# Kernel optimization log

Hardware: AMD Instinct MI355X
Metric: run time of the kernel (lower is better)

## Reference

```python
import jax, jax.numpy as jnp
import numpy as np

B, D = 8192, 1024
HR, HE, HF = 512, 4096, 2048
N_OPS, N_TASKS = 4, 4

def setup_inputs() -> dict:
    key = jax.random.key(0)
    ks = jax.random.split(key, 20)
    s = 0.02
    return {
        "x":        jax.random.normal(ks[0], (B, D), jnp.float32),
        # router
        "W_r1":   s*jax.random.normal(ks[1], (D, HR), jnp.float32),
        "b_r1":     jnp.zeros((HR,), jnp.float32),
        "W_dom":  s*jax.random.normal(ks[2], (HR, 2), jnp.float32),
        "b_dom":    jnp.zeros((2,), jnp.float32),
        "W_mop":  s*jax.random.normal(ks[3], (HR, N_OPS), jnp.float32),
        "W_lt":   s*jax.random.normal(ks[4], (HR, N_TASKS), jnp.float32),
        # math expert (operation hint = additive embedding)
        "op_emb": s*jax.random.normal(ks[5], (N_OPS, D), jnp.float32),
        "W_m1":   s*jax.random.normal(ks[6], (D, HE), jnp.float32),
        "b_m1":     jnp.zeros((HE,), jnp.float32),
        "W_m2":   s*jax.random.normal(ks[7], (HE, D), jnp.float32),
        "b_m2":     jnp.zeros((D,), jnp.float32),
        # language expert (task hint = additive embedding)
        "task_emb": s*jax.random.normal(ks[8], (N_TASKS, D), jnp.float32),
        "W_l1":   s*jax.random.normal(ks[9], (D, HE), jnp.float32),
        "b_l1":     jnp.zeros((HE,), jnp.float32),
        "W_l2":   s*jax.random.normal(ks[10], (HE, D), jnp.float32),
        "b_l2":     jnp.zeros((D,), jnp.float32),
        # fusion
        "W_f1":   s*jax.random.normal(ks[11], (D, HF), jnp.float32),
        "b_f1":     jnp.zeros((HF,), jnp.float32),
        "W_f2":   s*jax.random.normal(ks[12], (HF, D), jnp.float32),
        "b_f2":     jnp.zeros((D,), jnp.float32),
    }

def reference(x, W_r1, b_r1, W_dom, b_dom, W_mop, W_lt,
              op_emb, W_m1, b_m1, W_m2, b_m2,
              task_emb, W_l1, b_l1, W_l2, b_l2,
              W_f1, b_f1, W_f2, b_f2):
    # --- router ---
    h = jax.nn.relu(x @ W_r1 + b_r1)                      # [B, HR]
    dom_logits = h @ W_dom + b_dom                        # [B, 2]
    expert_weights = jax.nn.softmax(dom_logits, axis=-1)  # [B, 2]
    primary = jnp.argmax(dom_logits, axis=-1)             # [B]
    math_op = jnp.argmax(h @ W_mop, axis=-1)              # [B]
    lang_task = jnp.argmax(h @ W_lt, axis=-1)             # [B]
    # --- experts (vectorized equivalent of per-sample dispatch) ---
    math_in = x + op_emb[math_op]                         # [B, D]
    math_out = jax.nn.relu(math_in @ W_m1 + b_m1) @ W_m2 + b_m2
    lang_in = x + task_emb[lang_task]                     # [B, D]
    lang_out = jax.nn.relu(lang_in @ W_l1 + b_l1) @ W_l2 + b_l2
    selected = jnp.where((primary == 0)[:, None], math_out, lang_out)  # [B, D]
    # --- fusion: scale by routing weight of the chosen expert + MLP residual ---
    w = jnp.take_along_axis(expert_weights, primary[:, None], axis=1)  # [B, 1]
    fused = w * selected
    final = fused + jax.nn.relu(fused @ W_f1 + b_f1) @ W_f2 + b_f2     # [B, D]
    return final
```

## Files before the change

kernel.cpp:

```cpp
#include <hip/hip_runtime.h>
#include <hip/hip_bf16.h>
#include <stdint.h>

#define NB 8192
#define DD 1024
#define HRD 512
#define HED 4096
#define HFD 2048

typedef __attribute__((ext_vector_type(8))) short bf16x8;
typedef __attribute__((ext_vector_type(4))) float f32x4;
typedef unsigned short u16;

__device__ __forceinline__ u16 f2b(float f) {
    union { float f; uint32_t i; } c; c.f = f;
    uint32_t r = c.i + 0x7FFF + ((c.i >> 16) & 1);
    return (u16)(r >> 16);
}
__device__ __forceinline__ float b2f(u16 u) {
    union { uint32_t i; float f; } c; c.i = ((uint32_t)u) << 16; return c.f;
}

__device__ __forceinline__ void xcd_swz(int flat, int nwg, int nFast, int& f, int& s) {
    int xcd = flat & 7, rest = flat >> 3;
    int q = nwg >> 3, r = nwg & 7;
    int wg = (xcd < r ? xcd * (q + 1) : r * (q + 1) + (xcd - r) * q) + rest;
    f = wg % nFast; s = wg / nFast;
}

__global__ void k_init(int* cnt) { if (threadIdx.x < 2) cnt[threadIdx.x] = 0; }

__global__ __launch_bounds__(256) void k_split(const float4* __restrict__ x4,
                                               ushort4* __restrict__ hi4,
                                               ushort4* __restrict__ lo4) {
    int i = blockIdx.x * 256 + threadIdx.x;
    float4 v = x4[i];
    ushort4 h, l;
    h.x = f2b(v.x); l.x = f2b(v.x - b2f(h.x));
    h.y = f2b(v.y); l.y = f2b(v.y - b2f(h.y));
    h.z = f2b(v.z); l.z = f2b(v.z - b2f(h.z));
    h.w = f2b(v.w); l.w = f2b(v.w - b2f(h.w));
    hi4[i] = h; lo4[i] = l;
}

__global__ __launch_bounds__(256) void k_transpose(const float* __restrict__ in,
                                                   u16* __restrict__ out, int R, int C) {
    __shared__ float s[64][65];
    int tx = threadIdx.x & 63, ty = threadIdx.x >> 6;
    int c0 = blockIdx.x * 64, r0 = blockIdx.y * 64;
#pragma unroll
    for (int j = 0; j < 16; j++) { int r = ty + j * 4; s[r][tx] = in[(size_t)(r0 + r) * C + c0 + tx]; }
    __syncthreads();
#pragma unroll
    for (int j = 0; j < 16; j++) { int c = ty + j * 4; out[(size_t)(c0 + c) * R + r0 + tx] = f2b(s[tx][c]); }
}

__global__ __launch_bounds__(256) void k_transpose_split(const float* __restrict__ in,
                                                         u16* __restrict__ ohi, u16* __restrict__ olo,
                                                         int R, int C) {
    __shared__ float s[64][65];
    int tx = threadIdx.x & 63, ty = threadIdx.x >> 6;
    int c0 = blockIdx.x * 64, r0 = blockIdx.y * 64;
#pragma unroll
    for (int j = 0; j < 16; j++) { int r = ty + j * 4; s[r][tx] = in[(size_t)(r0 + r) * C + c0 + tx]; }
    __syncthreads();
#pragma unroll
    for (int j = 0; j < 16; j++) {
        int c = ty + j * 4;
        float v = s[tx][c];
        u16 h = f2b(v);
        ohi[(size_t)(c0 + c) * R + r0 + tx] = h;
        olo[(size_t)(c0 + c) * R + r0 + tx] = f2b(v - b2f(h));
    }
}

__device__ __forceinline__ void stage_tile(const char* gRowBase, long rowStrideBytes,
                                           u16* s, int tid) {
    int wave = tid >> 6, lane = tid & 63;
#pragma unroll
    for (int is = 0; is < 4; ++is) {
        int c = wave * 4 + is;
        int row = c * 8 + (lane >> 3);
        const char* g = gRowBase + (long)row * rowStrideBytes + (lane & 7) * 16;
        __builtin_amdgcn_global_load_lds(
            (const __attribute__((address_space(1))) void*)g,
            (__attribute__((address_space(3))) void*)((char*)s + c * 1024),
            16, 0, 0);
    }
}

__global__ __launch_bounds__(256) void k_router(const u16* __restrict__ Ah, const u16* __restrict__ Al,
                                                const u16* __restrict__ Bh, const u16* __restrict__ Bl,
                                                const float* __restrict__ bias, float* __restrict__ H) {
    __shared__ u16 sAh[2][128 * 64], sAl[2][128 * 64], sBh[2][128 * 64], sBl[2][128 * 64];
    int tid = threadIdx.x, lane = tid & 63, wave = tid >> 6;
    int flat = blockIdx.y * gridDim.x + blockIdx.x;
    int bm, bn;
    xcd_swz(flat, gridDim.x * gridDim.y, gridDim.x, bm, bn);
    f32x4 acc[4][4];
#pragma unroll
    for (int i = 0; i < 4; i++)
#pragma unroll
        for (int j = 0; j < 4; j++) acc[i][j] = (f32x4)0.f;
    int wm = (wave & 1) * 64, wn = (wave >> 1) * 64;
    const char* ahBase = (const char*)(Ah + (size_t)bm * 128 * DD);
    const char* alBase = (const char*)(Al + (size_t)bm * 128 * DD);
    const char* bhBase = (const char*)(Bh + (size_t)bn * 128 * DD);
    const char* blBase = (const char*)(Bl + (size_t)bn * 128 * DD);
    const int nk = DD / 64;
    stage_tile(ahBase, DD * 2, sAh[0], tid);
    stage_tile(alBase, DD * 2, sAl[0], tid);
    stage_tile(bhBase, DD * 2, sBh[0], tid);
    stage_tile(blBase, DD * 2, sBl[0], tid);
    asm volatile("s_waitcnt vmcnt(0)" ::: "memory");
    __builtin_amdgcn_s_barrier();
    int cur = 0;
    for (int it = 0; it < nk; ++it) {
        if (it + 1 < nk) {
            size_t ofs = (size_t)(it + 1) * 128;
            stage_tile(ahBase + ofs, DD * 2, sAh[cur ^ 1], tid);
            stage_tile(alBase + ofs, DD * 2, sAl[cur ^ 1], tid);
            stage_tile(bhBase + ofs, DD * 2, sBh[cur ^ 1], tid);
            stage_tile(blBase + ofs, DD * 2, sBl[cur ^ 1], tid);
        }
        const u16* pAh = sAh[cur]; const u16* pAl = sAl[cur];
        const u16* pBh = sBh[cur]; const u16* pBl = sBl[cur];
#pragma unroll
        for (int kk = 0; kk < 2; kk++) {
            int kofs = kk * 64 + (lane >> 4) * 16;
            bf16x8 vbh[4], vbl[4];
#pragma unroll
            for (int ni = 0; ni < 4; ni++) {
                int rB = (wn + ni * 16 + (lane & 15)) * 128 + kofs;
                vbh[ni] = *(const bf16x8*)((const char*)pBh + rB);
                vbl[ni] = *(const bf16x8*)((const char*)pBl + rB);
            }
#pragma unroll
            for (int mi = 0; mi < 4; mi++) {
                int rA = (wm + mi * 16 + (lane & 15)) * 128 + kofs;
                bf16x8 vah = *(const bf16x8*)((const char*)pAh + rA);
                bf16x8 val = *(const bf16x8*)((const char*)pAl + rA);
#pragma unroll
                for (int ni = 0; ni < 4; ni++) {
                    acc[mi][ni] = __builtin_amdgcn_mfma_f32_16x16x32_bf16(vah, vbh[ni], acc[mi][ni], 0, 0, 0);
                    acc[mi][ni] = __builtin_amdgcn_mfma_f32_16x16x32_bf16(vah, vbl[ni], acc[mi][ni], 0, 0, 0);
                    acc[mi][ni] = __builtin_amdgcn_mfma_f32_16x16x32_bf16(val, vbh[ni], acc[mi][ni], 0, 0, 0);
                }
            }
        }
        asm volatile("s_waitcnt vmcnt(0)" ::: "memory");
        __builtin_amdgcn_s_barrier();
        cur ^= 1;
    }
    int quad = lane >> 4, cl = lane & 15;
#pragma unroll
    for (int mi = 0; mi < 4; mi++)
#pragma unroll
        for (int r = 0; r < 4; r++) {
            int row = bm * 128 + wm + mi * 16 + quad * 4 + r;
#pragma unroll
            for (int ni = 0; ni < 4; ni++) {
                int col = bn * 128 + wn + ni * 16 + cl;
                float v = acc[mi][ni][r] + bias[col];
                H[(size_t)row * HRD + col] = fmaxf(v, 0.f);
            }
        }
}

__global__ __launch_bounds__(256) void k_heads(const float* __restrict__ H,
                                               const float* __restrict__ Wd, const float* __restrict__ bd,
                                               const float* __restrict__ Wm, const float* __restrict__ Wl,
                                               int* __restrict__ cnt, int* __restrict__ perm,
                                               float* __restrict__ wsc, int* __restrict__ eic) {
    int lane = threadIdx.x & 63, wave = threadIdx.x >> 6;
    int r = blockIdx.x * 4 + wave;
    const float4* h4 = (const float4*)(H + (size_t)r * HRD);
    float4 v0 = h4[lane * 2], v1 = h4[lane * 2 + 1];
    float hv[8] = {v0.x, v0.y, v0.z, v0.w, v1.x, v1.y, v1.z, v1.w};
    float a[10];
#pragma unroll
    for (int t = 0; t < 10; t++) a[t] = 0.f;
    int kbase = lane * 8;
#pragma unroll
    for (int j = 0; j < 8; j++) {
        int k = kbase + j;
        float h_ = hv[j];
        float2 wd = ((const float2*)Wd)[k];
        a[0] += h_ * wd.x; a[1] += h_ * wd.y;
        float4 wm = ((const float4*)Wm)[k];
        a[2] += h_ * wm.x; a[3] += h_ * wm.y; a[4] += h_ * wm.z; a[5] += h_ * wm.w;
        float4 wl = ((const float4*)Wl)[k];
        a[6] += h_ * wl.x; a[7] += h_ * wl.y; a[8] += h_ * wl.z; a[9] += h_ * wl.w;
    }
#pragma unroll
    for (int t = 0; t < 10; t++)
#pragma unroll
        for (int off = 32; off > 0; off >>= 1) a[t] += __shfl_down(a[t], off);
    if (lane == 0) {
        float d0 = a[0] + bd[0], d1 = a[1] + bd[1];
        int primary = (d1 > d0) ? 1 : 0;
        float w = 1.f / (1.f + expf(-fabsf(d0 - d1)));
        int mi = 0; float mv = a[2];
        if (a[3] > mv) { mv = a[3]; mi = 1; }
        if (a[4] > mv) { mv = a[4]; mi = 2; }
        if (a[5] > mv) { mv = a[5]; mi = 3; }
        int li = 0; float lv = a[6];
        if (a[7] > lv) { lv = a[7]; li = 1; }
        if (a[8] > lv) { lv = a[8]; li = 2; }
        int pos;
        if (a[9] > lv) { lv = a[9]; li = 3; }
        if (primary == 0) pos = atomicAdd(&cnt[0], 1);
        else              pos = NB - 1 - atomicAdd(&cnt[1], 1);
        perm[pos] = r; wsc[pos] = w; eic[pos] = (primary == 0) ? mi : li;
    }
}

__global__ __launch_bounds__(256) void k_gather(const float* __restrict__ x,
                                                const float* __restrict__ op_emb,
                                                const float* __restrict__ task_emb,
                                                const int* __restrict__ perm, const int* __restrict__ eic,
                                                const int* __restrict__ cnt, u16* __restrict__ xin) {
    int lane = threadIdx.x & 63, wave = threadIdx.x >> 6;
    int i = blockIdx.x * 4 + wave;
    int n0 = cnt[0];
    int r = perm[i];
    const float* emb = ((i >= n0) ? task_emb : op_emb) + (size_t)eic[i] * DD;
    const float4* x4 = (const float4*)(x + (size_t)r * DD);
    const float4* e4 = (const float4*)emb;
    ushort4* o4 = (ushort4*)(xin + (size_t)i * DD);
#pragma unroll
    for (int j = 0; j < 4; j++) {
        int idx = lane + j * 64;
        float4 xv = x4[idx], ev = e4[idx];
        ushort4 o;
        o.x = f2b(xv.x + ev.x); o.y = f2b(xv.y + ev.y);
        o.z = f2b(xv.z + ev.z); o.w = f2b(xv.w + ev.w);
        o4[idx] = o;
    }
}

template <int EPI>
__global__ __launch_bounds__(256) void k_gemm_dual(const u16* __restrict__ A,
                                                   const u16* __restrict__ Btm, const u16* __restrict__ Btl,
                                                   const float* __restrict__ biasm, const float* __restrict__ biasl,
                                                   u16* __restrict__ Out, int K, int N,
                                                   const int* __restrict__ cnt, const float* __restrict__ wsel) {
    __shared__ u16 sA[2][128 * 64];
    __shared__ u16 sB[2][128 * 64];
    int tid = threadIdx.x, lane = tid & 63, wave = tid >> 6;
    int flat = blockIdx.y * gridDim.x + blockIdx.x;
    int t, bn;
    xcd_swz(flat, gridDim.x * gridDim.y, gridDim.x, t, bn);
    int n0 = cnt[0];
    int tb = n0 >> 7;
    bool isMath = (t <= tb) && (t < 64);
    int tile = isMath ? t : (t - 1);
    int storeLo, storeHi;
    if (isMath) { storeLo = tile * 128; storeHi = n0 < storeLo + 128 ? n0 : storeLo + 128; }
    else        { storeHi = tile * 128 + 128; storeLo = n0 > tile * 128 ? n0 : tile * 128; }
    if (storeLo >= storeHi) return;
    const u16* Bt = isMath ? Btm : Btl;
    const float* bias = isMath ? biasm : biasl;
    f32x4 acc[4][4];
#pragma unroll
    for (int i = 0; i < 4; i++)
#pragma unroll
        for (int j = 0; j < 4; j++) acc[i][j] = (f32x4)0.f;
    int wm = (wave & 1) * 64, wn = (wave >> 1) * 64;
    const char* aBase = (const char*)(A + (size_t)tile * 128 * K);
    const char* bBase = (const char*)(Bt + (size_t)bn * 128 * K);
    const int nk = K >> 6;
    stage_tile(aBase, (long)K * 2, sA[0], tid);
    stage_tile(bBase, (long)K * 2, sB[0], tid);
    asm volatile("s_waitcnt vmcnt(0)" ::: "memory");
    __builtin_amdgcn_s_barrier();
    int cur = 0;
    for (int it = 0; it < nk; ++it) {
        if (it + 1 < nk) {
            size_t ofs = (size_t)(it + 1) * 128;
            stage_tile(aBase + ofs, (long)K * 2, sA[cur ^ 1], tid);
            stage_tile(bBase + ofs, (long)K * 2, sB[cur ^ 1], tid);
        }
        const u16* pA = sA[cur]; const u16* pB = sB[cur];
#pragma unroll
        for (int kk = 0; kk < 2; kk++) {
            int kofs = kk * 64 + (lane >> 4) * 16;
            bf16x8 vb[4];
#pragma unroll
            for (int ni = 0; ni < 4; ni++)
                vb[ni] = *(const bf16x8*)((const char*)pB + (wn + ni * 16 + (lane & 15)) * 128 + kofs);
#pragma unroll
            for (int mi = 0; mi < 4; mi++) {
                bf16x8 va = *(const bf16x8*)((const char*)pA + (wm + mi * 16 + (lane & 15)) * 128 + kofs);
#pragma unroll
                for (int ni = 0; ni < 4; ni++)
                    acc[mi][ni] = __builtin_amdgcn_mfma_f32_16x16x32_bf16(va, vb[ni], acc[mi][ni], 0, 0, 0);
            }
        }
        asm volatile("s_waitcnt vmcnt(0)" ::: "memory");
        __builtin_amdgcn_s_barrier();
        cur ^= 1;
    }
    int quad = lane >> 4, cl = lane & 15;
#pragma unroll
    for (int mi = 0; mi < 4; mi++)
#pragma unroll
        for (int r = 0; r < 4; r++) {
            int grow = tile * 128 + wm + mi * 16 + quad * 4 + r;
            if (grow < storeLo || grow >= storeHi) continue;
#pragma unroll
            for (int ni = 0; ni < 4; ni++) {
                int col = bn * 128 + wn + ni * 16 + cl;
                float v = acc[mi][ni][r] + bias[col];
                if constexpr (EPI == 0) {
                    Out[(size_t)grow * N + col] = f2b(fmaxf(v, 0.f));
                } else {
                    Out[(size_t)grow * N + col] = f2b(v * wsel[grow]);
                }
            }
        }
}

template <int EPI>
__global__ __launch_bounds__(256) void k_gemm_bt(const u16* __restrict__ A, const u16* __restrict__ Bt,
                                                 const float* __restrict__ bias, void* __restrict__ Out,
                                                 int K, int N,
                                                 const int* __restrict__ perm, const u16* __restrict__ resid) {
    __shared__ u16 sA[2][128 * 64];
    __shared__ u16 sB[2][128 * 64];
    int tid = threadIdx.x, lane = tid & 63, wave = tid >> 6;
    int flat = blockIdx.y * gridDim.x + blockIdx.x;
    int bm, bn;
    xcd_swz(flat, gridDim.x * gridDim.y, gridDim.x, bm, bn);
    f32x4 acc[4][4];
#pragma unroll
    for (int i = 0; i < 4; i++)
#pragma unroll
        for (int j = 0; j < 4; j++) acc[i][j] = (f32x4)0.f;
    int wm = (wave & 1) * 64, wn = (wave >> 1) * 64;
    const char* aBase = (const char*)(A + (size_t)bm * 128 * K);
    const char* bBase = (const char*)(Bt + (size_t)bn * 128 * K);
    const int nk = K >> 6;
    stage_tile(aBase, (long)K * 2, sA[0], tid);
    stage_tile(bBase, (long)K * 2, sB[0], tid);
    asm volatile("s_waitcnt vmcnt(0)" ::: "memory");
    __builtin_amdgcn_s_barrier();
    int cur = 0;
    for (int it = 0; it < nk; ++it) {
        if (it + 1 < nk) {
            size_t ofs = (size_t)(it + 1) * 128;
            stage_tile(aBase + ofs, (long)K * 2, sA[cur ^ 1], tid);
            stage_tile(bBase + ofs, (long)K * 2, sB[cur ^ 1], tid);
        }
        const u16* pA = sA[cur]; const u16* pB = sB[cur];
#pragma unroll
        for (int kk = 0; kk < 2; kk++) {
            int kofs = kk * 64 + (lane >> 4) * 16;
            bf16x8 vb[4];
#pragma unroll
            for (int ni = 0; ni < 4; ni++)
                vb[ni] = *(const bf16x8*)((const char*)pB + (wn + ni * 16 + (lane & 15)) * 128 + kofs);
#pragma unroll
            for (int mi = 0; mi < 4; mi++) {
                bf16x8 va = *(const bf16x8*)((const char*)pA + (wm + mi * 16 + (lane & 15)) * 128 + kofs);
#pragma unroll
                for (int ni = 0; ni < 4; ni++)
                    acc[mi][ni] = __builtin_amdgcn_mfma_f32_16x16x32_bf16(va, vb[ni], acc[mi][ni], 0, 0, 0);
            }
        }
        asm volatile("s_waitcnt vmcnt(0)" ::: "memory");
        __builtin_amdgcn_s_barrier();
        cur ^= 1;
    }
    int quad = lane >> 4, cl = lane & 15;
#pragma unroll
    for (int mi = 0; mi < 4; mi++)
#pragma unroll
        for (int r = 0; r < 4; r++) {
            int grow = bm * 128 + wm + mi * 16 + quad * 4 + r;
#pragma unroll
            for (int ni = 0; ni < 4; ni++) {
                int col = bn * 128 + wn + ni * 16 + cl;
                float v = acc[mi][ni][r] + bias[col];
                if constexpr (EPI == 0) {
                    ((u16*)Out)[(size_t)grow * N + col] = f2b(fmaxf(v, 0.f));
                } else {
                    v += b2f(resid[(size_t)grow * N + col]);
                    ((float*)Out)[(size_t)perm[grow] * N + col] = v;
                }
            }
        }
}

extern "C" void kernel_launch(void* const* d_in, const int* in_sizes, int n_in,
                              void* d_out, int out_size, void* d_ws, size_t ws_size,
                              hipStream_t stream) {
    const float* x      = (const float*)d_in[0];
    const float* W_r1   = (const float*)d_in[1];
    const float* b_r1   = (const float*)d_in[2];
    const float* W_dom  = (const float*)d_in[3];
    const float* b_dom  = (const float*)d_in[4];
    const float* W_mop  = (const float*)d_in[5];
    const float* W_lt   = (const float*)d_in[6];
    const float* op_emb = (const float*)d_in[7];
    const float* W_m1   = (const float*)d_in[8];
    const float* b_m1   = (const float*)d_in[9];
    const float* W_m2   = (const float*)d_in[10];
    const float* b_m2   = (const float*)d_in[11];
    const float* task_emb = (const float*)d_in[12];
    const float* W_l1   = (const float*)d_in[13];
    const float* b_l1   = (const float*)d_in[14];
    const float* W_l2   = (const float*)d_in[15];
    const float* b_l2   = (const float*)d_in[16];
    const float* W_f1   = (const float*)d_in[17];
    const float* b_f1   = (const float*)d_in[18];
    const float* W_f2   = (const float*)d_in[19];
    const float* b_f2   = (const float*)d_in[20];

    char* wsp = (char*)d_ws;
    size_t off = 0;
    auto take = [&](size_t bytes) -> char* {
        char* p = wsp + off;
        off += (bytes + 255) & ~(size_t)255;
        return p;
    };
    u16* Wr_hi = (u16*)take((size_t)HRD * DD * 2);
    u16* Wr_lo = (u16*)take((size_t)HRD * DD * 2);
    u16* Wm1t  = (u16*)take((size_t)HED * DD * 2);
    u16* Wl1t  = (u16*)take((size_t)HED * DD * 2);
    u16* Wm2t  = (u16*)take((size_t)DD * HED * 2);
    u16* Wl2t  = (u16*)take((size_t)DD * HED * 2);
    u16* Wf1t  = (u16*)take((size_t)HFD * DD * 2);
    u16* Wf2t  = (u16*)take((size_t)DD * HFD * 2);
    u16* x_hi  = (u16*)take((size_t)NB * DD * 2);
    u16* x_lo  = (u16*)take((size_t)NB * DD * 2);
    float* Hbuf = (float*)take((size_t)NB * HRD * 4);
    u16* hid   = (u16*)take((size_t)NB * HED * 2);
    int* cnt   = (int*)take(256);
    int* perm  = (int*)take(NB * 4);
    int* eic   = (int*)take(NB * 4);
    float* wsc = (float*)take(NB * 4);
    u16* xin   = x_hi;
    u16* fused = x_lo;
    u16* hid2  = Wm1t;

    k_init<<<1, 64, 0, stream>>>(cnt);
    k_split<<<(NB * DD / 4) / 256, 256, 0, stream>>>((const float4*)x, (ushort4*)x_hi, (ushort4*)x_lo);
    k_transpose_split<<<dim3(HRD / 64, DD / 64), 256, 0, stream>>>(W_r1, Wr_hi, Wr_lo, DD, HRD);
    k_transpose<<<dim3(HED / 64, DD / 64), 256, 0, stream>>>(W_m1, Wm1t, DD, HED);
    k_transpose<<<dim3(HED / 64, DD / 64), 256, 0, stream>>>(W_l1, Wl1t, DD, HED);
    k_transpose<<<dim3(DD / 64, HED / 64), 256, 0, stream>>>(W_m2, Wm2t, HED, DD);
    k_transpose<<<dim3(DD / 64, HED / 64), 256, 0, stream>>>(W_l2, Wl2t, HED, DD);
    k_transpose<<<dim3(HFD / 64, DD / 64), 256, 0, stream>>>(W_f1, Wf1t, DD, HFD);
    k_transpose<<<dim3(DD / 64, HFD / 64), 256, 0, stream>>>(W_f2, Wf2t, HFD, DD);

    k_router<<<dim3(NB / 128, HRD / 128), 256, 0, stream>>>(x_hi, x_lo, Wr_hi, Wr_lo, b_r1, Hbuf);
    k_heads<<<NB / 4, 256, 0, stream>>>(Hbuf, W_dom, b_dom, W_mop, W_lt, cnt, perm, wsc, eic);
    k_gather<<<NB / 4, 256, 0, stream>>>(x, op_emb, task_emb, perm, eic, cnt, xin);

    k_gemm_dual<0><<<dim3(NB / 128 + 1, HED / 128), 256, 0, stream>>>(
        xin, Wm1t, Wl1t, b_m1, b_l1, hid, DD, HED, cnt, nullptr);
    k_gemm_dual<1><<<dim3(NB / 128 + 1, DD / 128), 256, 0, stream>>>(
        hid, Wm2t, Wl2t, b_m2, b_l2, fused, HED, DD, cnt, wsc);
    k_gemm_bt<0><<<dim3(NB / 128, HFD / 128), 256, 0, stream>>>(
        fused, Wf1t, b_f1, hid2, DD, HFD, nullptr, nullptr);
    k_gemm_bt<2><<<dim3(NB / 128, DD / 128), 256, 0, stream>>>(
        hid2, Wf2t, b_f2, d_out, HFD, DD, perm, fused);
}
```

Before: 747.2 us.

## Use 256x128 GEMM tiles with triple-buffered direct-to-LDS loads and padded routing gap

Result: slower. 811.2 us (+8.6%).

```diff
diff --git a/kernel.cpp b/kernel.cpp
--- a/kernel.cpp
+++ b/kernel.cpp
@@ -3,6 +3,8 @@
 #include <stdint.h>
 
 #define NB 8192
+#define NBPAD 8448
+#define NT 33
 #define DD 1024
 #define HRD 512
 #define HED 4096
@@ -210,7 +212,7 @@
         int pos;
         if (a[9] > lv) { lv = a[9]; li = 3; }
         if (primary == 0) pos = atomicAdd(&cnt[0], 1);
-        else              pos = NB - 1 - atomicAdd(&cnt[1], 1);
+        else              pos = NBPAD - 1 - atomicAdd(&cnt[1], 1);
         perm[pos] = r; wsc[pos] = w; eic[pos] = (primary == 0) ? mi : li;
     }
 }
@@ -223,6 +225,7 @@
     int lane = threadIdx.x & 63, wave = threadIdx.x >> 6;
     int i = blockIdx.x * 4 + wave;
     int n0 = cnt[0];
+    if (i >= n0 && i < n0 + 256) return;
     int r = perm[i];
     const float* emb = ((i >= n0) ? task_emb : op_emb) + (size_t)eic[i] * DD;
     const float4* x4 = (const float4*)(x + (size_t)r * DD);
@@ -239,151 +242,122 @@
     }
 }
 
-template <int EPI>
-__global__ __launch_bounds__(256) void k_gemm_dual(const u16* __restrict__ A,
-                                                   const u16* __restrict__ Btm, const u16* __restrict__ Btl,
-                                                   const float* __restrict__ biasm, const float* __restrict__ biasl,
-                                                   u16* __restrict__ Out, int K, int N,
-                                                   const int* __restrict__ cnt, const float* __restrict__ wsel) {
-    __shared__ u16 sA[2][128 * 64];
-    __shared__ u16 sB[2][128 * 64];
+template <int EPI, bool DUAL>
+__global__ __launch_bounds__(512) void k_gemm256(
+    const u16* __restrict__ A, const u16* __restrict__ B0, const u16* __restrict__ B1,
+    const float* __restrict__ bias0, const float* __restrict__ bias1,
+    void* __restrict__ Out, int K, int N,
+    const int* __restrict__ cnt, const float* __restrict__ wsel,
+    const int* __restrict__ perm, const u16* __restrict__ resid) {
+    __shared__ __align__(16) u16 sA[3][256 * 64];
+    __shared__ __align__(16) u16 sB[3][128 * 64];
     int tid = threadIdx.x, lane = tid & 63, wave = tid >> 6;
     int flat = blockIdx.y * gridDim.x + blockIdx.x;
     int t, bn;
     xcd_swz(flat, gridDim.x * gridDim.y, gridDim.x, t, bn);
     int n0 = cnt[0];
-    int tb = n0 >> 7;
-    bool isMath = (t <= tb) && (t < 64);
-    int tile = isMath ? t : (t - 1);
-    int storeLo, storeHi;
-    if (isMath) { storeLo = tile * 128; storeHi = n0 < storeLo + 128 ? n0 : storeLo + 128; }
-    else        { storeHi = tile * 128 + 128; storeLo = n0 > tile * 128 ? n0 : tile * 128; }
-    if (storeLo >= storeHi) return;
-    const u16* Bt = isMath ? Btm : Btl;
-    const float* bias = isMath ? biasm : biasl;
+    const u16* Bt; const float* bias; int storeLo, storeHi;
+    if constexpr (DUAL) {
+        int rowLo = t * 256;
+        if (rowLo < n0) {
+            Bt = B0; bias = bias0;
+            storeLo = rowLo; storeHi = (n0 < rowLo + 256) ? n0 : rowLo + 256;
+        } else {
+            Bt = B1; bias = bias1;
+            storeLo = (rowLo > n0 + 256) ? rowLo : n0 + 256; storeHi = rowLo + 256;
+            if (storeLo >= storeHi) return;
+        }
+    } else {
+        Bt = B0; bias = bias0; storeLo = 0; storeHi = 0x7fffffff;
+    }
     f32x4 acc[4][4];
 #pragma unroll
     for (int i = 0; i < 4; i++)
 #pragma unroll
         for (int j = 0; j < 4; j++) acc[i][j] = (f32x4)0.f;
-    int wm = (wave & 1) * 64, wn = (wave >> 1) * 64;
-    const char* aBase = (const char*)(A + (size_t)tile * 128 * K);
+    int wm = (wave & 3) * 64, wn = (wave >> 2) * 64;
+    const long strideB = (long)K * 2;
+    const char* aBase = (const char*)(A + (size_t)t * 256 * K);
     const char* bBase = (const char*)(Bt + (size_t)bn * 128 * K);
+    const int srcCol = (((lane & 7) ^ ((lane >> 3) & 7)) << 4);
+    const int laneRow = lane >> 3;
     const int nk = K >> 6;
-    stage_tile(aBase, (long)K * 2, sA[0], tid);
-    stage_tile(bBase, (long)K * 2, sB[0], tid);
-    asm volatile("s_waitcnt vmcnt(0)" ::: "memory");
-    __builtin_amdgcn_s_barrier();
-    int cur = 0;
-    for (int it = 0; it < nk; ++it) {
-        if (it + 1 < nk) {
-            size_t ofs = (size_t)(it + 1) * 128;
-            stage_tile(aBase + ofs, (long)K * 2, sA[cur ^ 1], tid);
-            stage_tile(bBase + ofs, (long)K * 2, sB[cur ^ 1], tid);
-        }
-        const u16* pA = sA[cur]; const u16* pB = sB[cur];
+
+    auto stageA = [&](int j, int slot) {
+#pragma unroll
+        for (int ic = 0; ic < 4; ic++) {
+            int c = wave * 4 + ic;
+            const char* g = aBase + (long)(c * 8 + laneRow) * strideB + j * 128 + srcCol;
+            __builtin_amdgcn_global_load_lds(
+                (const __attribute__((address_space(1))) void*)g,
+                (__attribute__((address_space(3))) void*)((char*)&sA[slot][0] + c * 1024),
+                16, 0, 0);
+        }
+    };
+    auto stageB = [&](int j, int slot) {
+#pragma unroll
+        for (int ic = 0; ic < 2; ic++) {
+            int c = wave * 2 + ic;
+            const char* g = bBase + (long)(c * 8 + laneRow) * strideB + j * 128 + srcCol;
+            __builtin_amdgcn_global_load_lds(
+                (const __attribute__((address_space(1))) void*)g,
+                (__attribute__((address_space(3))) void*)((char*)&sB[slot][0] + c * 1024),
+                16, 0, 0);
+        }
+    };
+
+    stageA(0, 0); stageB(0, 0);
+    stageA(1, 1); stageB(1, 1);
+    int sc = 0, sn = 2;
+    for (int j = 0; j < nk; ++j) {
+        if (j + 2 < nk) {
+            stageA(j + 2, sn); stageB(j + 2, sn);
+            asm volatile("s_waitcnt vmcnt(12)" ::: "memory");
+        } else if (j + 1 < nk) {
+            asm volatile("s_waitcnt vmcnt(6)" ::: "memory");
+        } else {
+            asm volatile("s_waitcnt vmcnt(0)" ::: "memory");
+        }
+        __builtin_amdgcn_s_barrier();
+        const char* pA = (const char*)&sA[sc][0];
+        const char* pB = (const char*)&sB[sc][0];
 #pragma unroll
         for (int kk = 0; kk < 2; kk++) {
-            int kofs = kk * 64 + (lane >> 4) * 16;
-            bf16x8 vb[4];
+            int u = (((kk * 4 + (lane >> 4)) ^ (lane & 7)) << 4);
+            bf16x8 va[4], vb[4];
 #pragma unroll
             for (int ni = 0; ni < 4; ni++)
-                vb[ni] = *(const bf16x8*)((const char*)pB + (wn + ni * 16 + (lane & 15)) * 128 + kofs);
-#pragma unroll
-            for (int mi = 0; mi < 4; mi++) {
-                bf16x8 va = *(const bf16x8*)((const char*)pA + (wm + mi * 16 + (lane & 15)) * 128 + kofs);
+                vb[ni] = *(const bf16x8*)(pB + (wn + ni * 16 + (lane & 15)) * 128 + u);
+#pragma unroll
+            for (int mi = 0; mi < 4; mi++)
+                va[mi] = *(const bf16x8*)(pA + (wm + mi * 16 + (lane & 15)) * 128 + u);
+#pragma unroll
+            for (int mi = 0; mi < 4; mi++)
 #pragma unroll
                 for (int ni = 0; ni < 4; ni++)
-                    acc[mi][ni] = __builtin_amdgcn_mfma_f32_16x16x32_bf16(va, vb[ni], acc[mi][ni], 0, 0, 0);
-            }
-        }
-        asm volatile("s_waitcnt vmcnt(0)" ::: "memory");
+                    acc[mi][ni] = __builtin_amdgcn_mfma_f32_16x16x32_bf16(va[mi], vb[ni], acc[mi][ni], 0, 0, 0);
+        }
+        asm volatile("" ::: "memory");
         __builtin_amdgcn_s_barrier();
-        cur ^= 1;
+        sc = (sc == 2) ? 0 : sc + 1;
+        sn = (sn == 2) ? 0 : sn + 1;
     }
     int quad = lane >> 4, cl = lane & 15;
 #pragma unroll
     for (int mi = 0; mi < 4; mi++)
 #pragma unroll
         for (int r = 0; r < 4; r++) {
-            int grow = tile * 128 + wm + mi * 16 + quad * 4 + r;
+            int grow = t * 256 + wm + mi * 16 + quad * 4 + r;
             if (grow < storeLo || grow >= storeHi) continue;
-#pragma unroll
-            for (int ni = 0; ni < 4; ni++) {
-                int col = bn * 128 + wn + ni * 16 + cl;
-                float v = acc[mi][ni][r] + bias[col];
-                if constexpr (EPI == 0) {
-                    Out[(size_t)grow * N + col] = f2b(fmaxf(v, 0.f));
-                } else {
-                    Out[(size_t)grow * N + col] = f2b(v * wsel[grow]);
-                }
-            }
-        }
-}
-
-template <int EPI>
-__global__ __launch_bounds__(256) void k_gemm_bt(const u16* __restrict__ A, const u16* __restrict__ Bt,
-                                                 const float* __restrict__ bias, void* __restrict__ Out,
-                                                 int K, int N,
-                                                 const int* __restrict__ perm, const u16* __restrict__ resid) {
-    __shared__ u16 sA[2][128 * 64];
-    __shared__ u16 sB[2][128 * 64];
-    int tid = threadIdx.x, lane = tid & 63, wave = tid >> 6;
-    int flat = blockIdx.y * gridDim.x + blockIdx.x;
-    int bm, bn;
-    xcd_swz(flat, gridDim.x * gridDim.y, gridDim.x, bm, bn);
-    f32x4 acc[4][4];
-#pragma unroll
-    for (int i = 0; i < 4; i++)
-#pragma unroll
-        for (int j = 0; j < 4; j++) acc[i][j] = (f32x4)0.f;
-    int wm = (wave & 1) * 64, wn = (wave >> 1) * 64;
-    const char* aBase = (const char*)(A + (size_t)bm * 128 * K);
-    const char* bBase = (const char*)(Bt + (size_t)bn * 128 * K);
-    const int nk = K >> 6;
-    stage_tile(aBase, (long)K * 2, sA[0], tid);
-    stage_tile(bBase, (long)K * 2, sB[0], tid);
-    asm volatile("s_waitcnt vmcnt(0)" ::: "memory");
-    __builtin_amdgcn_s_barrier();
-    int cur = 0;
-    for (int it = 0; it < nk; ++it) {
-        if (it + 1 < nk) {
-            size_t ofs = (size_t)(it + 1) * 128;
-            stage_tile(aBase + ofs, (long)K * 2, sA[cur ^ 1], tid);
-            stage_tile(bBase + ofs, (long)K * 2, sB[cur ^ 1], tid);
-        }
-        const u16* pA = sA[cur]; const u16* pB = sB[cur];
-#pragma unroll
-        for (int kk = 0; kk < 2; kk++) {
-            int kofs = kk * 64 + (lane >> 4) * 16;
-            bf16x8 vb[4];
-#pragma unroll
-            for (int ni = 0; ni < 4; ni++)
-                vb[ni] = *(const bf16x8*)((const char*)pB + (wn + ni * 16 + (lane & 15)) * 128 + kofs);
-#pragma unroll
-            for (int mi = 0; mi < 4; mi++) {
-                bf16x8 va = *(const bf16x8*)((const char*)pA + (wm + mi * 16 + (lane & 15)) * 128 + kofs);
-#pragma unroll
-                for (int ni = 0; ni < 4; ni++)
-                    acc[mi][ni] = __builtin_amdgcn_mfma_f32_16x16x32_bf16(va, vb[ni], acc[mi][ni], 0, 0, 0);
-            }
-        }
-        asm volatile("s_waitcnt vmcnt(0)" ::: "memory");
-        __builtin_amdgcn_s_barrier();
-        cur ^= 1;
-    }
-    int quad = lane >> 4, cl = lane & 15;
-#pragma unroll
-    for (int mi = 0; mi < 4; mi++)
-#pragma unroll
-        for (int r = 0; r < 4; r++) {
-            int grow = bm * 128 + wm + mi * 16 + quad * 4 + r;
+            if constexpr (EPI == 2) { if (grow >= n0 && grow < n0 + 256) continue; }
 #pragma unroll
             for (int ni = 0; ni < 4; ni++) {
                 int col = bn * 128 + wn + ni * 16 + cl;
                 float v = acc[mi][ni][r] + bias[col];
                 if constexpr (EPI == 0) {
                     ((u16*)Out)[(size_t)grow * N + col] = f2b(fmaxf(v, 0.f));
+                } else if constexpr (EPI == 1) {
+                    ((u16*)Out)[(size_t)grow * N + col] = f2b(v * wsel[grow]);
                 } else {
                     v += b2f(resid[(size_t)grow * N + col]);
                     ((float*)Out)[(size_t)perm[grow] * N + col] = v;
@@ -430,19 +404,20 @@
     u16* Wl1t  = (u16*)take((size_t)HED * DD * 2);
     u16* Wm2t  = (u16*)take((size_t)DD * HED * 2);
     u16* Wl2t  = (u16*)take((size_t)DD * HED * 2);
+    (void)take((size_t)2 * 1024 * 1024);
     u16* Wf1t  = (u16*)take((size_t)HFD * DD * 2);
     u16* Wf2t  = (u16*)take((size_t)DD * HFD * 2);
-    u16* x_hi  = (u16*)take((size_t)NB * DD * 2);
-    u16* x_lo  = (u16*)take((size_t)NB * DD * 2);
-    float* Hbuf = (float*)take((size_t)NB * HRD * 4);
-    u16* hid   = (u16*)take((size_t)NB * HED * 2);
+    u16* x_hi  = (u16*)take((size_t)NBPAD * DD * 2);
+    u16* x_lo  = (u16*)take((size_t)NBPAD * DD * 2);
+    u16* hid   = (u16*)take((size_t)NBPAD * HED * 2);
     int* cnt   = (int*)take(256);
-    int* perm  = (int*)take(NB * 4);
-    int* eic   = (int*)take(NB * 4);
-    float* wsc = (float*)take(NB * 4);
-    u16* xin   = x_hi;
-    u16* fused = x_lo;
-    u16* hid2  = Wm1t;
+    int* perm  = (int*)take(NBPAD * 4);
+    int* eic   = (int*)take(NBPAD * 4);
+    float* wsc = (float*)take(NBPAD * 4);
+    u16* xin    = x_hi;
+    u16* fused  = x_lo;
+    u16* hid2   = Wm1t;
+    float* Hbuf = (float*)hid;
 
     k_init<<<1, 64, 0, stream>>>(cnt);
     k_split<<<(NB * DD / 4) / 256, 256, 0, stream>>>((const float4*)x, (ushort4*)x_hi, (ushort4*)x_lo);
@@ -456,14 +431,14 @@
 
     k_router<<<dim3(NB / 128, HRD / 128), 256, 0, stream>>>(x_hi, x_lo, Wr_hi, Wr_lo, b_r1, Hbuf);
     k_heads<<<NB / 4, 256, 0, stream>>>(Hbuf, W_dom, b_dom, W_mop, W_lt, cnt, perm, wsc, eic);
-    k_gather<<<NB / 4, 256, 0, stream>>>(x, op_emb, task_emb, perm, eic, cnt, xin);
-
-    k_gemm_dual<0><<<dim3(NB / 128 + 1, HED / 128), 256, 0, stream>>>(
-        xin, Wm1t, Wl1t, b_m1, b_l1, hid, DD, HED, cnt, nullptr);
-    k_gemm_dual<1><<<dim3(NB / 128 + 1, DD / 128), 256, 0, stream>>>(
-        hid, Wm2t, Wl2t, b_m2, b_l2, fused, HED, DD, cnt, wsc);
-    k_gemm_bt<0><<<dim3(NB / 128, HFD / 128), 256, 0, stream>>>(
-        fused, Wf1t, b_f1, hid2, DD, HFD, nullptr, nullptr);
-    k_gemm_bt<2><<<dim3(NB / 128, DD / 128), 256, 0, stream>>>(
-        hid2, Wf2t, b_f2, d_out, HFD, DD, perm, fused);
-}
+    k_gather<<<NBPAD / 4, 256, 0, stream>>>(x, op_emb, task_emb, perm, eic, cnt, xin);
+
+    k_gemm256<0, true><<<dim3(NT, HED / 128), 512, 0, stream>>>(
+        xin, Wm1t, Wl1t, b_m1, b_l1, hid, DD, HED, cnt, nullptr, nullptr, nullptr);
+    k_gemm256<1, true><<<dim3(NT, DD / 128), 512, 0, stream>>>(
+        hid, Wm2t, Wl2t, b_m2, b_l2, fused, HED, DD, cnt, wsc, nullptr, nullptr);
+    k_gemm256<0, false><<<dim3(NT, HFD / 128), 512, 0, stream>>>(
+        fused, Wf1t, nullptr, b_f1, nullptr, hid2, DD, HFD, cnt, nullptr, nullptr, nullptr);
+    k_gemm256<2, false><<<dim3(NT, DD / 128), 512, 0, stream>>>(
+        hid2, Wf2t, nullptr, b_f2, nullptr, d_out, HFD, DD, cnt, nullptr, perm, fused);
+}
```
